# Kernel tuning notes

Hardware: AMD Instinct MI355X
Metric: run time of the kernel (lower is better)

## Reference

```python
import jax, jax.numpy as jnp
import numpy as np

IN_FEATURES = 256
OUT_FEATURES = 64
ALPHA = 0.2  # leaky relu slope


def _xavier_uniform(key, shape, gain=1.414):
    fan_in, fan_out = shape[0], shape[1]
    limit = gain * np.sqrt(6.0 / (fan_in + fan_out))
    return jax.random.uniform(key, shape, jnp.float32, -limit, limit)


def setup_inputs() -> dict:
    key = jax.random.key(0)
    k_h, k_W, k_a = jax.random.split(key, 3)
    h = jax.random.normal(k_h, (8, 2048, IN_FEATURES), dtype=jnp.float32)
    W = _xavier_uniform(k_W, (IN_FEATURES, OUT_FEATURES))
    a = _xavier_uniform(k_a, (2 * OUT_FEATURES, 1))
    return {"h": h, "W": W, "a": a}


def reference(h, W, a):
    # h: [B, N, F_in], W: [F_in, D], a: [2D, 1]
    Wh = h @ W  # [B, N, D]
    D = Wh.shape[-1]
    a1 = a[:D, 0]   # attends to source node i (repeat_interleave side)
    a2 = a[D:, 0]   # attends to target node j (repeat side)
    f1 = Wh @ a1    # [B, N]
    f2 = Wh @ a2    # [B, N]
    # e[b, i, j] = leakyrelu(a1.Wh[b,i] + a2.Wh[b,j])  -- identical math to
    # the original's O(N^2 * 2D) repeat/concat, without materializing it.
    e = jax.nn.leaky_relu(f1[:, :, None] + f2[:, None, :], negative_slope=ALPHA)  # [B, N, N]
    # NOTE: original applies softmax over dim=1 (over i, per column j).
    attention = jax.nn.softmax(e, axis=1)  # [B, N, N]
    # dropout is identity in eval mode
    h_prime = jnp.einsum('bij,bjd->bid', attention, Wh)  # [B, N, D]
    return jax.nn.elu(h_prime)  # concat=True path
```

## Files before the change

### kernel.cpp

```cpp
#include <hip/hip_runtime.h>

#define B 8
#define N 2048
#define KF 256
#define DF 64
#define LOG2E 1.44269504088896340736f
#define NR 2049

typedef __attribute__((ext_vector_type(8))) short short8;
typedef __attribute__((ext_vector_type(4))) float float4v;

__device__ __forceinline__ float fexp2(float x) {
#if __has_builtin(__builtin_amdgcn_exp2f)
    return __builtin_amdgcn_exp2f(x);
#else
    return exp2f(x);
#endif
}
__device__ __forceinline__ float eluf(float x) {
    return x > 0.f ? x : fexp2(x * LOG2E) - 1.0f;
}
__device__ __forceinline__ short bf16r(float x) {
    unsigned u = __float_as_uint(x);
    return (short)((u + 0x8000u) >> 16);
}
#define DOT4(c, u, p) \
    p = fmaf(c.x, u.x, fmaf(c.y, u.y, fmaf(c.z, u.z, fmaf(c.w, u.w, p))));

__global__ __launch_bounds__(256) void k_wh(const float* __restrict__ h,
                                            const float* __restrict__ W,
                                            const float* __restrict__ a,
                                            float* __restrict__ Wh,
                                            float* __restrict__ f1,
                                            float* __restrict__ f2) {
    __shared__ __align__(16) unsigned char smem[34816];
    short* lwt  = (short*)smem;
    float* lv   = (float*)(smem + 32768);
    float* lred = (float*)smem;
    float* lp   = (float*)(smem + 16896);

    int t = threadIdx.x;
    int wv = t >> 6, lane = t & 63;
    int n15 = lane & 15, q = lane >> 4;
    int bx = blockIdx.x;

    const float* hr = h + ((long)bx * 32 + n15) * KF + wv * 64 + q * 8;
    float4 c0 = *(const float4*)(hr);
    float4 c1 = *(const float4*)(hr + 4);
    float4 c2 = *(const float4*)(hr + 32);
    float4 c3 = *(const float4*)(hr + 36);

    {
        const float4* wr4 = (const float4*)(W + t * DF);
        float s1 = 0.f, s2 = 0.f;
        #pragma unroll
        for (int c = 0; c < 16; c++) {
            float4 w4 = wr4[c];
            float4 a1v = *(const float4*)(a + 4 * c);
            float4 a2v = *(const float4*)(a + DF + 4 * c);
            lwt[(4 * c + 0) * 256 + t] = bf16r(w4.x);
            lwt[(4 * c + 1) * 256 + t] = bf16r(w4.y);
            lwt[(4 * c + 2) * 256 + t] = bf16r(w4.z);
            lwt[(4 * c + 3) * 256 + t] = bf16r(w4.w);
            s1 = fmaf(w4.x, a1v.x, fmaf(w4.y, a1v.y, fmaf(w4.z, a1v.z, fmaf(w4.w, a1v.w, s1))));
            s2 = fmaf(w4.x, a2v.x, fmaf(w4.y, a2v.y, fmaf(w4.z, a2v.z, fmaf(w4.w, a2v.w, s2))));
        }
        lv[t] = s1;
        lv[256 + t] = s2;
    }
    __syncthreads();

    const short* bq = lwt + n15 * 256 + wv * 64 + q * 8;
    short8 s0b0 = *(const short8*)(bq);
    short8 s0b1 = *(const short8*)(bq + 16 * 256);
    short8 s0b2 = *(const short8*)(bq + 32 * 256);
    short8 s0b3 = *(const short8*)(bq + 48 * 256);
    short8 s1b0 = *(const short8*)(bq + 32);
    short8 s1b1 = *(const short8*)(bq + 16 * 256 + 32);
    short8 s1b2 = *(const short8*)(bq + 32 * 256 + 32);
    short8 s1b3 = *(const short8*)(bq + 48 * 256 + 32);
    const float* vv = lv + wv * 64 + q * 8;
    float4 u00 = *(const float4*)(vv);
    float4 u01 = *(const float4*)(vv + 4);
    float4 u10 = *(const float4*)(vv + 32);
    float4 u11 = *(const float4*)(vv + 36);
    float4 x00 = *(const float4*)(vv + 256);
    float4 x01 = *(const float4*)(vv + 256 + 4);
    float4 x10 = *(const float4*)(vv + 256 + 32);
    float4 x11 = *(const float4*)(vv + 256 + 36);
    __syncthreads();

    #pragma unroll
    for (int rt = 0; rt < 2; rt++) {
        float4 m0, m1, m2, m3;
        if (rt < 1) {
            const float* hn = hr + 16 * KF;
            m0 = *(const float4*)(hn);
            m1 = *(const float4*)(hn + 4);
            m2 = *(const float4*)(hn + 32);
            m3 = *(const float4*)(hn + 36);
        }
        float p1 = 0.f, p2 = 0.f;
        DOT4(c0, u00, p1) DOT4(c1, u01, p1) DOT4(c2, u10, p1) DOT4(c3, u11, p1)
        DOT4(c0, x00, p2) DOT4(c1, x01, p2) DOT4(c2, x10, p2) DOT4(c3, x11, p2)

        short8 af0 = { bf16r(c0.x), bf16r(c0.y), bf16r(c0.z), bf16r(c0.w),
                       bf16r(c1.x), bf16r(c1.y), bf16r(c1.z), bf16r(c1.w) };
        short8 af1 = { bf16r(c2.x), bf16r(c2.y), bf16r(c2.z), bf16r(c2.w),
                       bf16r(c3.x), bf16r(c3.y), bf16r(c3.z), bf16r(c3.w) };
        float4v acc0 = {0.f, 0.f, 0.f, 0.f}, acc1 = acc0, acc2 = acc0, acc3 = acc0;
        acc0 = __builtin_amdgcn_mfma_f32_16x16x32_bf16(af0, s0b0, acc0, 0, 0, 0);
        acc0 = __builtin_amdgcn_mfma_f32_16x16x32_bf16(af1, s1b0, acc0, 0, 0, 0);
        acc1 = __builtin_amdgcn_mfma_f32_16x16x32_bf16(af0, s0b1, acc1, 0, 0, 0);
        acc1 = __builtin_amdgcn_mfma_f32_16x16x32_bf16(af1, s1b1, acc1, 0, 0, 0);
        acc2 = __builtin_amdgcn_mfma_f32_16x16x32_bf16(af0, s0b2, acc2, 0, 0, 0);
        acc2 = __builtin_amdgcn_mfma_f32_16x16x32_bf16(af1, s1b2, acc2, 0, 0, 0);
        acc3 = __builtin_amdgcn_mfma_f32_16x16x32_bf16(af0, s0b3, acc3, 0, 0, 0);
        acc3 = __builtin_amdgcn_mfma_f32_16x16x32_bf16(af1, s1b3, acc3, 0, 0, 0);

        #define STASH(nb, A)                                                  \
            {                                                                 \
                _Pragma("unroll")                                             \
                for (int r = 0; r < 4; r++)                                   \
                    lred[wv * 1056 + (q * 4 + r) * 66 + nb * 16 + n15] = A[r]; \
            }
        STASH(0, acc0) STASH(1, acc1) STASH(2, acc2) STASH(3, acc3)
        #undef STASH
        p1 += __shfl_xor(p1, 16, 64); p1 += __shfl_xor(p1, 32, 64);
        p2 += __shfl_xor(p2, 16, 64); p2 += __shfl_xor(p2, 32, 64);
        if (q == 0) { lp[wv * 16 + n15] = p1; lp[64 + wv * 16 + n15] = p2; }
        __syncthreads();

        long i0 = (long)bx * 32 + rt * 16;
        int d = t & 63, ig = t >> 6;
        int bb = (int)(i0 >> 11);
        int il = (int)(i0 & (N - 1));
        float s0 = 0.f, s1 = 0.f, s2 = 0.f, s3 = 0.f;
        #pragma unroll
        for (int w = 0; w < 4; w++) {
            const float* lr = lred + w * 1056 + (ig * 4) * 66 + d;
            s0 += lr[0]; s1 += lr[66]; s2 += lr[132]; s3 += lr[198];
        }
        float* wp = Wh + ((long)bb * N + il + ig * 4) * DF + d;
        wp[0]      = s0;
        wp[DF]     = s1;
        wp[2 * DF] = s2;
        wp[3 * DF] = s3;

        if (t < 16) {
            f1[i0 + t] = lp[t] + lp[16 + t] + lp[32 + t] + lp[48 + t];
        } else if (t < 32) {
            int tt = t + 48;
            f2[i0 + t - 16] = lp[tt] + lp[16 + tt] + lp[32 + tt] + lp[48 + tt];
        }
        __syncthreads();
        c0 = m0; c1 = m1; c2 = m2; c3 = m3;
    }
}

__global__ __launch_bounds__(512) void k_rank(const float* __restrict__ f1,
                                              const float* __restrict__ f2,
                                              int* __restrict__ tIdx,
                                              int* __restrict__ si,
                                              float* __restrict__ gA,
                                              float* __restrict__ gsA) {
    __shared__ __align__(16) float4 qv[2048];
    __shared__ unsigned u2[2048];
    __shared__ float rS1[8][64], rS1s[8][64];
    __shared__ int   rC2[8][64], rC3[8][64];

    int t = threadIdx.x;
    int b = blockIdx.y;
    int base = blockIdx.x * 64;
    const float* f1g = f1 + b * N;
    const float* f2g = f2 + b * N;

    #pragma unroll
    for (int r = 0; r < 4; r++) {
        int idx = t + r * 512;
        float v1 = f1g[idx], v2 = f2g[idx];
        qv[idx] = make_float4(v1, fexp2(v1 * LOG2E), fexp2(v1 * 0.2f * LOG2E), v2);
        unsigned ub = __float_as_uint(v2);
        u2[idx] = ub ^ (((unsigned)((int)ub >> 31)) | 0x80000000u);
    }
    __syncthreads();

    int jl = t & 63, qt = t >> 6;
    int j = base + jl;
    float4 qj = qv[j];
    unsigned uj = u2[j];
    float negf2 = -qj.w, negf1 = -qj.x;
    int c2 = 0, c3 = 0;
    float S1 = 0.f, S1s = 0.f;
    int p0 = qt * 256;
    #pragma unroll 4
    for (int p = p0; p < p0 + 256; p++) {
        float4 qa = qv[p];
        unsigned up = u2[p];
        c2 += (up < uj || (up == uj && p < j)) ? 1 : 0;
        bool c = qa.x < negf2;
        S1  += c ? 0.f : qa.y;
        S1s += c ? qa.z : 0.f;
        c3 += (qa.w < negf1) ? 1 : 0;
    }
    rC2[qt][jl] = c2; rC3[qt][jl] = c3;
    rS1[qt][jl] = S1; rS1s[qt][jl] = S1s;
    __syncthreads();

    if (t < 64) {
        int j2 = base + t;
        float4 qj2 = qv[j2];
        int rank = 0, ti = 0;
        float s1 = 0.f, s1s = 0.f;
        #pragma unroll
        for (int k = 0; k < 8; k++) {
            rank += rC2[k][t]; ti += rC3[k][t];
            s1 += rS1[k][t];   s1s += rS1s[k][t];
        }
        float E2  = fexp2(qj2.w * LOG2E);
        float E2s = fexp2(qj2.w * 0.2f * LOG2E);
        float rr = 1.0f / (E2 * s1 + E2s * s1s);
        tIdx[b * N + j2] = ti;
        si [b * N + rank] = j2;
        gA [b * N + rank] = E2 * rr;
        gsA[b * N + rank] = E2s * rr;
    }
}

__global__ __launch_bounds__(256) void k_seg(const float* __restrict__ Wh,
                                             const int* __restrict__ si,
                                             const float* __restrict__ gA,
                                             const float* __restrict__ gsA,
                                             float* __restrict__ segG,
                                             float* __restrict__ segGs) {
    int t = threadIdx.x;
    int d = t & 63, sq = t >> 6;
    int seg = blockIdx.x * 4 + sq, b = blockIdx.y;
    const int*   sib = si  + b * N;
    const float* ga  = gA  + b * N;
    const float* gsa = gsA + b * N;
    const float* whb = Wh + (((long)b) << 11) * DF;
    float sg = 0.f, sgs = 0.f;
    #pragma unroll 8
    for (int x = 0; x < 32; x++) {
        int p = seg * 32 + x;
        int r = sib[p];
        float wv = whb[r * DF + d];
        sg  = fmaf(ga[p],  wv, sg);
        sgs = fmaf(gsa[p], wv, sgs);
    }
    segG [(b * 64 + seg) * DF + d] = sg;
    segGs[(b * 64 + seg) * DF + d] = sgs;
}

__global__ __launch_bounds__(256) void k_tab(const float* __restrict__ Wh,
                                             const int* __restrict__ si,
                                             const float* __restrict__ gA,
                                             const float* __restrict__ gsA,
                                             const float* __restrict__ segG,
                                             const float* __restrict__ segGs,
                                             float* __restrict__ SSg,
                                             float* __restrict__ PSgs) {
    __shared__ float lPG[4][64], lPGs[4][64];
    __shared__ float lTG[4][64], lTGs[4][64];
    __shared__ float wG[4][64],  wGs[4][64];
    int t = threadIdx.x;
    int d = t & 63, sub = t >> 6;
    int seg = blockIdx.x, b = blockIdx.y;

    const float* sgb  = segG  + (b * 64) * DF + d;
    const float* sgsb = segGs + (b * 64) * DF + d;
    float pg = 0.f, pgs = 0.f, tg = 0.f, tgs = 0.f;
    #pragma unroll
    for (int k = 0; k < 16; k++) {
        int s = sub * 16 + k;
        float vg = sgb[s * DF], vgs = sgsb[s * DF];
        tg += vg; tgs += vgs;
        if (s < seg) { pg += vg; pgs += vgs; }
    }
    lPG[sub][d] = pg; lPGs[sub][d] = pgs;
    lTG[sub][d] = tg; lTGs[sub][d] = tgs;

    int p0 = seg * 32 + sub * 8;
    const int*   sib = si  + b * N;
    const float* ga  = gA  + b * N;
    const float* gsa = gsA + b * N;
    const float* whb = Wh + (((long)b) << 11) * DF;
    float rows[8], gv[8], gsv[8];
    float sg = 0.f, sgs = 0.f;
    #pragma unroll
    for (int x = 0; x < 8; x++) {
        int p = p0 + x;
        int r = sib[p];
        float wv = whb[r * DF + d];
        rows[x] = wv; gv[x] = ga[p]; gsv[x] = gsa[p];
        sg  = fmaf(gv[x],  wv, sg);
        sgs = fmaf(gsv[x], wv, sgs);
    }
    wG[sub][d] = sg; wGs[sub][d] = sgs;
    __syncthreads();

    float totG  = lTG[0][d] + lTG[1][d] + lTG[2][d] + lTG[3][d];
    float totGs = lTGs[0][d] + lTGs[1][d] + lTGs[2][d] + lTGs[3][d];
    float baseG  = lPG[0][d] + lPG[1][d] + lPG[2][d] + lPG[3][d];
    float baseGs = lPGs[0][d] + lPGs[1][d] + lPGs[2][d] + lPGs[3][d];
    #pragma unroll
    for (int k = 0; k < 3; k++) {
        if (k < sub) { baseG += wG[k][d]; baseGs += wGs[k][d]; }
    }

    float* ssb = SSg  + ((long)b * NR) * DF + d;
    float* psb = PSgs + ((long)b * NR) * DF + d;
    float rg = baseG, rgs = baseGs;
    #pragma unroll
    for (int x = 0; x < 8; x++) {
        long p = p0 + x;
        ssb[p * DF] = totG - rg;
        psb[p * DF] = rgs;
        rg  = fmaf(gv[x],  rows[x], rg);
        rgs = fmaf(gsv[x], rows[x], rgs);
    }
    if (seg == 63 && sub == 3) {
        ssb[2048L * DF] = 0.f;
        psb[2048L * DF] = rgs;
    }
}

__global__ __launch_bounds__(256) void k_out(const float* __restrict__ f1,
                                             const int* __restrict__ tIdx,
                                             const float* __restrict__ SSg,
                                             const float* __restrict__ PSgs,
                                             float* __restrict__ out) {
    int t = threadIdx.x;
    int b = blockIdx.y;
    int i0 = blockIdx.x * 64;
    int rr = t >> 6, d = t & 63;
    const float* sgB = SSg  + ((long)b * NR) * DF + d;
    const float* pgB = PSgs + ((long)b * NR) * DF + d;
    float* ob = out + ((long)b * N + i0) * DF + d;
    #pragma unroll
    for (int kk = 0; kk < 16; kk++) {
        int r = rr + kk * 4;
        int ti = tIdx[b * N + i0 + r];
        float v = f1[b * N + i0 + r];
        float e1  = fexp2(v * LOG2E);
        float e1s = fexp2(v * 0.2f * LOG2E);
        float x = e1 * sgB[(long)ti * DF] + e1s * pgB[(long)ti * DF];
        ob[(long)r * DF] = eluf(x);
    }
}

extern "C" void kernel_launch(void* const* d_in, const int* in_sizes, int n_in,
                              void* d_out, int out_size, void* d_ws, size_t ws_size,
                              hipStream_t stream) {
    const float* h = (const float*)d_in[0];
    const float* W = (const float*)d_in[1];
    const float* a = (const float*)d_in[2];
    float* out = (float*)d_out;

    char* ws = (char*)d_ws;
    const size_t NB = (size_t)B * N;
    size_t off = 0;
    float* Wh    = (float*)(ws + off); off += NB * DF * sizeof(float);
    float* f1    = (float*)(ws + off); off += NB * sizeof(float);
    float* f2    = (float*)(ws + off); off += NB * sizeof(float);
    int*   tIdx  = (int*)  (ws + off); off += NB * sizeof(int);
    int*   si    = (int*)  (ws + off); off += NB * sizeof(int);
    float* gA    = (float*)(ws + off); off += NB * sizeof(float);
    float* gsA   = (float*)(ws + off); off += NB * sizeof(float);
    float* segG  = (float*)(ws + off); off += (size_t)B * 64 * DF * sizeof(float);
    float* segGs = (float*)(ws + off); off += (size_t)B * 64 * DF * sizeof(float);
    float* SSg   = (float*)(ws + off); off += (size_t)B * NR * DF * sizeof(float);
    float* PSgs  = (float*)(ws + off); off += (size_t)B * NR * DF * sizeof(float);
    (void)off; (void)ws_size;

    k_wh  <<<NB / 32, 256, 0, stream>>>(h, W, a, Wh, f1, f2);
    k_rank<<<dim3(N / 64, B), 512, 0, stream>>>(f1, f2, tIdx, si, gA, gsA);
    k_seg <<<dim3(16, B), 256, 0, stream>>>(Wh, si, gA, gsA, segG, segGs);
    k_tab <<<dim3(64, B), 256, 0, stream>>>(Wh, si, gA, gsA, segG, segGs, SSg, PSgs);
    k_out <<<dim3(N / 64, B), 256, 0, stream>>>(f1, tIdx, SSg, PSgs, out);
}
```

Before: 101.6 us.

## Fuse segment sums, prefix tables and output into one kernel

```diff
diff --git a/kernel.cpp b/kernel.cpp
--- a/kernel.cpp
+++ b/kernel.cpp
@@ -5,7 +5,6 @@
 #define KF 256
 #define DF 64
 #define LOG2E 1.44269504088896340736f
-#define NR 2049
 
 typedef __attribute__((ext_vector_type(8))) short short8;
 typedef __attribute__((ext_vector_type(4))) float float4v;
@@ -227,126 +226,80 @@
     }
 }
 
-__global__ __launch_bounds__(256) void k_seg(const float* __restrict__ Wh,
+__global__ __launch_bounds__(256) void k_fin(const float* __restrict__ Wh,
+                                             const float* __restrict__ f1,
+                                             const int* __restrict__ tIdx,
                                              const int* __restrict__ si,
                                              const float* __restrict__ gA,
                                              const float* __restrict__ gsA,
-                                             float* __restrict__ segG,
-                                             float* __restrict__ segGs) {
+                                             float* __restrict__ out) {
+    __shared__ int   lsi[2048];
+    __shared__ float lg[2048], lgs[2048];
+    __shared__ float pG[65][64], pGs[65][64];
+    __shared__ float e1v[64], e1sv[64];
+    __shared__ int   tv[64];
+
     int t = threadIdx.x;
-    int d = t & 63, sq = t >> 6;
-    int seg = blockIdx.x * 4 + sq, b = blockIdx.y;
-    const int*   sib = si  + b * N;
-    const float* ga  = gA  + b * N;
-    const float* gsa = gsA + b * N;
+    int d = t & 63, q = t >> 6;
+    int b = blockIdx.y, base = blockIdx.x * 64;
     const float* whb = Wh + (((long)b) << 11) * DF;
-    float sg = 0.f, sgs = 0.f;
-    #pragma unroll 8
-    for (int x = 0; x < 32; x++) {
-        int p = seg * 32 + x;
-        int r = sib[p];
-        float wv = whb[r * DF + d];
-        sg  = fmaf(ga[p],  wv, sg);
-        sgs = fmaf(gsa[p], wv, sgs);
-    }
-    segG [(b * 64 + seg) * DF + d] = sg;
-    segGs[(b * 64 + seg) * DF + d] = sgs;
-}
-
-__global__ __launch_bounds__(256) void k_tab(const float* __restrict__ Wh,
-                                             const int* __restrict__ si,
-                                             const float* __restrict__ gA,
-                                             const float* __restrict__ gsA,
-                                             const float* __restrict__ segG,
-                                             const float* __restrict__ segGs,
-                                             float* __restrict__ SSg,
-                                             float* __restrict__ PSgs) {
-    __shared__ float lPG[4][64], lPGs[4][64];
-    __shared__ float lTG[4][64], lTGs[4][64];
-    __shared__ float wG[4][64],  wGs[4][64];
-    int t = threadIdx.x;
-    int d = t & 63, sub = t >> 6;
-    int seg = blockIdx.x, b = blockIdx.y;
-
-    const float* sgb  = segG  + (b * 64) * DF + d;
-    const float* sgsb = segGs + (b * 64) * DF + d;
-    float pg = 0.f, pgs = 0.f, tg = 0.f, tgs = 0.f;
+
     #pragma unroll
-    for (int k = 0; k < 16; k++) {
-        int s = sub * 16 + k;
-        float vg = sgb[s * DF], vgs = sgsb[s * DF];
-        tg += vg; tgs += vgs;
-        if (s < seg) { pg += vg; pgs += vgs; }
-    }
-    lPG[sub][d] = pg; lPGs[sub][d] = pgs;
-    lTG[sub][d] = tg; lTGs[sub][d] = tgs;
-
-    int p0 = seg * 32 + sub * 8;
-    const int*   sib = si  + b * N;
-    const float* ga  = gA  + b * N;
-    const float* gsa = gsA + b * N;
-    const float* whb = Wh + (((long)b) << 11) * DF;
-    float rows[8], gv[8], gsv[8];
-    float sg = 0.f, sgs = 0.f;
-    #pragma unroll
-    for (int x = 0; x < 8; x++) {
-        int p = p0 + x;
-        int r = sib[p];
-        float wv = whb[r * DF + d];
-        rows[x] = wv; gv[x] = ga[p]; gsv[x] = gsa[p];
-        sg  = fmaf(gv[x],  wv, sg);
-        sgs = fmaf(gsv[x], wv, sgs);
-    }
-    wG[sub][d] = sg; wGs[sub][d] = sgs;
-    __syncthreads();
-
-    float totG  = lTG[0][d] + lTG[1][d] + lTG[2][d] + lTG[3][d];
-    float totGs = lTGs[0][d] + lTGs[1][d] + lTGs[2][d] + lTGs[3][d];
-    float baseG  = lPG[0][d] + lPG[1][d] + lPG[2][d] + lPG[3][d];
-    float baseGs = lPGs[0][d] + lPGs[1][d] + lPGs[2][d] + lPGs[3][d];
-    #pragma unroll
-    for (int k = 0; k < 3; k++) {
-        if (k < sub) { baseG += wG[k][d]; baseGs += wGs[k][d]; }
-    }
-
-    float* ssb = SSg  + ((long)b * NR) * DF + d;
-    float* psb = PSgs + ((long)b * NR) * DF + d;
-    float rg = baseG, rgs = baseGs;
-    #pragma unroll
-    for (int x = 0; x < 8; x++) {
-        long p = p0 + x;
-        ssb[p * DF] = totG - rg;
-        psb[p * DF] = rgs;
-        rg  = fmaf(gv[x],  rows[x], rg);
-        rgs = fmaf(gsv[x], rows[x], rgs);
-    }
-    if (seg == 63 && sub == 3) {
-        ssb[2048L * DF] = 0.f;
-        psb[2048L * DF] = rgs;
-    }
-}
-
-__global__ __launch_bounds__(256) void k_out(const float* __restrict__ f1,
-                                             const int* __restrict__ tIdx,
-                                             const float* __restrict__ SSg,
-                                             const float* __restrict__ PSgs,
-                                             float* __restrict__ out) {
-    int t = threadIdx.x;
-    int b = blockIdx.y;
-    int i0 = blockIdx.x * 64;
-    int rr = t >> 6, d = t & 63;
-    const float* sgB = SSg  + ((long)b * NR) * DF + d;
-    const float* pgB = PSgs + ((long)b * NR) * DF + d;
-    float* ob = out + ((long)b * N + i0) * DF + d;
-    #pragma unroll
-    for (int kk = 0; kk < 16; kk++) {
-        int r = rr + kk * 4;
-        int ti = tIdx[b * N + i0 + r];
-        float v = f1[b * N + i0 + r];
-        float e1  = fexp2(v * LOG2E);
-        float e1s = fexp2(v * 0.2f * LOG2E);
-        float x = e1 * sgB[(long)ti * DF] + e1s * pgB[(long)ti * DF];
-        ob[(long)r * DF] = eluf(x);
+    for (int r = 0; r < 8; r++) {
+        int p = t + r * 256;
+        lsi[p] = si[b * N + p];
+        lg[p]  = gA[b * N + p];
+        lgs[p] = gsA[b * N + p];
+    }
+    if (t < 64) {
+        int row = base + t;
+        float v = f1[b * N + row];
+        e1v[t]  = fexp2(v * LOG2E);
+        e1sv[t] = fexp2(v * 0.2f * LOG2E);
+        tv[t]   = tIdx[b * N + row];
+        pG[0][t] = 0.f; pGs[0][t] = 0.f;
+    }
+    __syncthreads();
+
+    #pragma unroll 1
+    for (int s = 0; s < 16; s++) {
+        int seg = q * 16 + s;
+        float sg = 0.f, sgs = 0.f;
+        #pragma unroll 8
+        for (int x = 0; x < 32; x++) {
+            int p = seg * 32 + x;
+            float w = whb[lsi[p] * DF + d];
+            sg  = fmaf(lg[p],  w, sg);
+            sgs = fmaf(lgs[p], w, sgs);
+        }
+        pG[seg + 1][d] = sg;
+        pGs[seg + 1][d] = sgs;
+    }
+    __syncthreads();
+    if (q == 0) {
+        float run = 0.f;
+        for (int s = 1; s <= 64; s++) { run += pG[s][d]; pG[s][d] = run; }
+    } else if (q == 1) {
+        float run = 0.f;
+        for (int s = 1; s <= 64; s++) { run += pGs[s][d]; pGs[s][d] = run; }
+    }
+    __syncthreads();
+
+    float TG = pG[64][d];
+    #pragma unroll 1
+    for (int rr = 0; rr < 16; rr++) {
+        int r = q * 16 + rr;
+        int ti = tv[r];
+        int s = ti >> 5, e = ti & 31, p0 = s * 32;
+        float pg = pG[s][d], pgs = pGs[s][d];
+        for (int x = 0; x < e; x++) {
+            int p = p0 + x;
+            float w = whb[lsi[p] * DF + d];
+            pg  = fmaf(lg[p],  w, pg);
+            pgs = fmaf(lgs[p], w, pgs);
+        }
+        float o = e1v[r] * (TG - pg) + e1sv[r] * pgs;
+        out[((long)b * N + base + r) * DF + d] = eluf(o);
     }
 }
 
@@ -361,22 +314,16 @@
     char* ws = (char*)d_ws;
     const size_t NB = (size_t)B * N;
     size_t off = 0;
-    float* Wh    = (float*)(ws + off); off += NB * DF * sizeof(float);
-    float* f1    = (float*)(ws + off); off += NB * sizeof(float);
-    float* f2    = (float*)(ws + off); off += NB * sizeof(float);
-    int*   tIdx  = (int*)  (ws + off); off += NB * sizeof(int);
-    int*   si    = (int*)  (ws + off); off += NB * sizeof(int);
-    float* gA    = (float*)(ws + off); off += NB * sizeof(float);
-    float* gsA   = (float*)(ws + off); off += NB * sizeof(float);
-    float* segG  = (float*)(ws + off); off += (size_t)B * 64 * DF * sizeof(float);
-    float* segGs = (float*)(ws + off); off += (size_t)B * 64 * DF * sizeof(float);
-    float* SSg   = (float*)(ws + off); off += (size_t)B * NR * DF * sizeof(float);
-    float* PSgs  = (float*)(ws + off); off += (size_t)B * NR * DF * sizeof(float);
+    float* Wh   = (float*)(ws + off); off += NB * DF * sizeof(float);
+    float* f1   = (float*)(ws + off); off += NB * sizeof(float);
+    float* f2   = (float*)(ws + off); off += NB * sizeof(float);
+    int*   tIdx = (int*)  (ws + off); off += NB * sizeof(int);
+    int*   si   = (int*)  (ws + off); off += NB * sizeof(int);
+    float* gA   = (float*)(ws + off); off += NB * sizeof(float);
+    float* gsA  = (float*)(ws + off); off += NB * sizeof(float);
     (void)off; (void)ws_size;
 
     k_wh  <<<NB / 32, 256, 0, stream>>>(h, W, a, Wh, f1, f2);
     k_rank<<<dim3(N / 64, B), 512, 0, stream>>>(f1, f2, tIdx, si, gA, gsA);
-    k_seg <<<dim3(16, B), 256, 0, stream>>>(Wh, si, gA, gsA, segG, segGs);
-    k_tab <<<dim3(64, B), 256, 0, stream>>>(Wh, si, gA, gsA, segG, segGs, SSg, PSgs);
-    k_out <<<dim3(N / 64, B), 256, 0, stream>>>(f1, tIdx, SSg, PSgs, out);
-}
+    k_fin <<<dim3(N / 64, B), 256, 0, stream>>>(Wh, f1, tIdx, si, gA, gsA, out);
+}
```

New measurement: 140.9 us. 1.39x slower.

## Fuse segment reduction into rank kernel via atomics and precompute packed sort keys

Applied to the files above, without the earlier changes.

```diff
diff --git a/kernel.cpp b/kernel.cpp
--- a/kernel.cpp
+++ b/kernel.cpp
@@ -24,6 +24,10 @@
     unsigned u = __float_as_uint(x);
     return (short)((u + 0x8000u) >> 16);
 }
+__device__ __forceinline__ unsigned sortkey(float x) {
+    unsigned u = __float_as_uint(x);
+    return u ^ (((unsigned)((int)u >> 31)) | 0x80000000u);
+}
 #define DOT4(c, u, p) \
     p = fmaf(c.x, u.x, fmaf(c.y, u.y, fmaf(c.z, u.z, fmaf(c.w, u.w, p))));
 
@@ -32,7 +36,9 @@
                                             const float* __restrict__ a,
                                             float* __restrict__ Wh,
                                             float* __restrict__ f1,
-                                            float* __restrict__ f2) {
+                                            float* __restrict__ f2,
+                                            float4* __restrict__ qpack,
+                                            float* __restrict__ segzero) {
     __shared__ __align__(16) unsigned char smem[34816];
     short* lwt  = (short*)smem;
     float* lv   = (float*)(smem + 32768);
@@ -43,6 +49,8 @@
     int wv = t >> 6, lane = t & 63;
     int n15 = lane & 15, q = lane >> 4;
     int bx = blockIdx.x;
+
+    if (t < 128) segzero[bx * 128 + t] = 0.f;
 
     const float* hr = h + ((long)bx * 32 + n15) * KF + wv * 64 + q * 8;
     float4 c0 = *(const float4*)(hr);
@@ -148,7 +156,15 @@
         wp[3 * DF] = s3;
 
         if (t < 16) {
-            f1[i0 + t] = lp[t] + lp[16 + t] + lp[32 + t] + lp[48 + t];
+            float v1 = lp[t] + lp[16 + t] + lp[32 + t] + lp[48 + t];
+            f1[i0 + t] = v1;
+            float v2 = lp[64 + t] + lp[80 + t] + lp[96 + t] + lp[112 + t];
+            float4 qe;
+            qe.x = __uint_as_float(sortkey(v1));
+            qe.y = __uint_as_float(sortkey(v2));
+            qe.z = fexp2(v1 * LOG2E);
+            qe.w = fexp2(v1 * 0.2f * LOG2E);
+            qpack[i0 + t] = qe;
         } else if (t < 32) {
             int tt = t + 48;
             f2[i0 + t - 16] = lp[tt] + lp[16 + tt] + lp[32 + tt] + lp[48 + tt];
@@ -158,58 +174,54 @@
     }
 }
 
-__global__ __launch_bounds__(512) void k_rank(const float* __restrict__ f1,
+__global__ __launch_bounds__(512) void k_rank(const float4* __restrict__ qpack,
+                                              const float* __restrict__ f1,
                                               const float* __restrict__ f2,
+                                              const float* __restrict__ Wh,
                                               int* __restrict__ tIdx,
                                               int* __restrict__ si,
                                               float* __restrict__ gA,
-                                              float* __restrict__ gsA) {
-    __shared__ __align__(16) float4 qv[2048];
-    __shared__ unsigned u2[2048];
+                                              float* __restrict__ gsA,
+                                              float* __restrict__ segG,
+                                              float* __restrict__ segGs) {
     __shared__ float rS1[8][64], rS1s[8][64];
     __shared__ int   rC2[8][64], rC3[8][64];
+    __shared__ float gL[64], gsL[64];
+    __shared__ int   rkL[64];
 
     int t = threadIdx.x;
-    int b = blockIdx.y;
-    int base = blockIdx.x * 64;
-    const float* f1g = f1 + b * N;
-    const float* f2g = f2 + b * N;
-
-    #pragma unroll
-    for (int r = 0; r < 4; r++) {
-        int idx = t + r * 512;
-        float v1 = f1g[idx], v2 = f2g[idx];
-        qv[idx] = make_float4(v1, fexp2(v1 * LOG2E), fexp2(v1 * 0.2f * LOG2E), v2);
-        unsigned ub = __float_as_uint(v2);
-        u2[idx] = ub ^ (((unsigned)((int)ub >> 31)) | 0x80000000u);
-    }
-    __syncthreads();
-
-    int jl = t & 63, qt = t >> 6;
+    int b = blockIdx.y, base = blockIdx.x * 64;
+    int jl = t & 63;
     int j = base + jl;
-    float4 qj = qv[j];
-    unsigned uj = u2[j];
-    float negf2 = -qj.w, negf1 = -qj.x;
+    float f1j = f1[(long)b * N + j];
+    float f2j = f2[(long)b * N + j];
+    unsigned u2j = sortkey(f2j);
+    unsigned long long Kj = (((unsigned long long)u2j) << 32) | (unsigned)j;
+    unsigned vkNf2 = sortkey(-f2j);
+    unsigned vkNf1 = sortkey(-f1j);
+
+    int qt = __builtin_amdgcn_readfirstlane(t >> 6);
+    const float4* qp = qpack + (long)b * N + qt * 256;
     int c2 = 0, c3 = 0;
     float S1 = 0.f, S1s = 0.f;
-    int p0 = qt * 256;
-    #pragma unroll 4
-    for (int p = p0; p < p0 + 256; p++) {
-        float4 qa = qv[p];
-        unsigned up = u2[p];
-        c2 += (up < uj || (up == uj && p < j)) ? 1 : 0;
-        bool c = qa.x < negf2;
-        S1  += c ? 0.f : qa.y;
-        S1s += c ? qa.z : 0.f;
-        c3 += (qa.w < negf1) ? 1 : 0;
+    #pragma unroll 8
+    for (int x = 0; x < 256; x++) {
+        float4 e = qp[x];
+        unsigned u1p = __float_as_uint(e.x);
+        unsigned u2p = __float_as_uint(e.y);
+        unsigned long long Kp = (((unsigned long long)u2p) << 32)
+                              | (unsigned)(qt * 256 + x);
+        c2 += (Kp < Kj) ? 1 : 0;
+        c3 += (u2p < vkNf1) ? 1 : 0;
+        bool cc = u1p < vkNf2;
+        S1  += cc ? 0.f : e.z;
+        S1s += cc ? e.w : 0.f;
     }
     rC2[qt][jl] = c2; rC3[qt][jl] = c3;
     rS1[qt][jl] = S1; rS1s[qt][jl] = S1s;
     __syncthreads();
 
     if (t < 64) {
-        int j2 = base + t;
-        float4 qj2 = qv[j2];
         int rank = 0, ti = 0;
         float s1 = 0.f, s1s = 0.f;
         #pragma unroll
@@ -217,40 +229,29 @@
             rank += rC2[k][t]; ti += rC3[k][t];
             s1 += rS1[k][t];   s1s += rS1s[k][t];
         }
-        float E2  = fexp2(qj2.w * LOG2E);
-        float E2s = fexp2(qj2.w * 0.2f * LOG2E);
+        float E2  = fexp2(f2j * LOG2E);
+        float E2s = fexp2(f2j * 0.2f * LOG2E);
         float rr = 1.0f / (E2 * s1 + E2s * s1s);
-        tIdx[b * N + j2] = ti;
-        si [b * N + rank] = j2;
-        gA [b * N + rank] = E2 * rr;
-        gsA[b * N + rank] = E2s * rr;
-    }
-}
-
-__global__ __launch_bounds__(256) void k_seg(const float* __restrict__ Wh,
-                                             const int* __restrict__ si,
-                                             const float* __restrict__ gA,
-                                             const float* __restrict__ gsA,
-                                             float* __restrict__ segG,
-                                             float* __restrict__ segGs) {
-    int t = threadIdx.x;
-    int d = t & 63, sq = t >> 6;
-    int seg = blockIdx.x * 4 + sq, b = blockIdx.y;
-    const int*   sib = si  + b * N;
-    const float* ga  = gA  + b * N;
-    const float* gsa = gsA + b * N;
+        float g = E2 * rr, gs = E2s * rr;
+        tIdx[(long)b * N + j] = ti;
+        si [(long)b * N + rank] = j;
+        gA [(long)b * N + rank] = g;
+        gsA[(long)b * N + rank] = gs;
+        rkL[t] = rank; gL[t] = g; gsL[t] = gs;
+    }
+    __syncthreads();
+
+    int d = t & 63, rg = t >> 6;
     const float* whb = Wh + (((long)b) << 11) * DF;
-    float sg = 0.f, sgs = 0.f;
-    #pragma unroll 8
-    for (int x = 0; x < 32; x++) {
-        int p = seg * 32 + x;
-        int r = sib[p];
-        float wv = whb[r * DF + d];
-        sg  = fmaf(ga[p],  wv, sg);
-        sgs = fmaf(gsa[p], wv, sgs);
-    }
-    segG [(b * 64 + seg) * DF + d] = sg;
-    segGs[(b * 64 + seg) * DF + d] = sgs;
+    #pragma unroll
+    for (int r = 0; r < 8; r++) {
+        int lr = rg * 8 + r;
+        int row = base + lr;
+        float w = whb[row * DF + d];
+        int seg = rkL[lr] >> 5;
+        atomicAdd(&segG [(b * 64 + seg) * DF + d], gL[lr] * w);
+        atomicAdd(&segGs[(b * 64 + seg) * DF + d], gsL[lr] * w);
+    }
 }
 
 __global__ __launch_bounds__(256) void k_tab(const float* __restrict__ Wh,
@@ -301,7 +302,6 @@
     __syncthreads();
 
     float totG  = lTG[0][d] + lTG[1][d] + lTG[2][d] + lTG[3][d];
-    float totGs = lTGs[0][d] + lTGs[1][d] + lTGs[2][d] + lTGs[3][d];
     float baseG  = lPG[0][d] + lPG[1][d] + lPG[2][d] + lPG[3][d];
     float baseGs = lPGs[0][d] + lPGs[1][d] + lPGs[2][d] + lPGs[3][d];
     #pragma unroll
@@ -361,22 +361,22 @@
     char* ws = (char*)d_ws;
     const size_t NB = (size_t)B * N;
     size_t off = 0;
-    float* Wh    = (float*)(ws + off); off += NB * DF * sizeof(float);
-    float* f1    = (float*)(ws + off); off += NB * sizeof(float);
-    float* f2    = (float*)(ws + off); off += NB * sizeof(float);
-    int*   tIdx  = (int*)  (ws + off); off += NB * sizeof(int);
-    int*   si    = (int*)  (ws + off); off += NB * sizeof(int);
-    float* gA    = (float*)(ws + off); off += NB * sizeof(float);
-    float* gsA   = (float*)(ws + off); off += NB * sizeof(float);
-    float* segG  = (float*)(ws + off); off += (size_t)B * 64 * DF * sizeof(float);
-    float* segGs = (float*)(ws + off); off += (size_t)B * 64 * DF * sizeof(float);
-    float* SSg   = (float*)(ws + off); off += (size_t)B * NR * DF * sizeof(float);
-    float* PSgs  = (float*)(ws + off); off += (size_t)B * NR * DF * sizeof(float);
+    float*  Wh    = (float*) (ws + off); off += NB * DF * sizeof(float);
+    float*  f1    = (float*) (ws + off); off += NB * sizeof(float);
+    float*  f2    = (float*) (ws + off); off += NB * sizeof(float);
+    int*    tIdx  = (int*)   (ws + off); off += NB * sizeof(int);
+    int*    si    = (int*)   (ws + off); off += NB * sizeof(int);
+    float*  gA    = (float*) (ws + off); off += NB * sizeof(float);
+    float*  gsA   = (float*) (ws + off); off += NB * sizeof(float);
+    float4* qpack = (float4*)(ws + off); off += NB * sizeof(float4);
+    float*  segG  = (float*) (ws + off); off += (size_t)B * 64 * DF * sizeof(float);
+    float*  segGs = (float*) (ws + off); off += (size_t)B * 64 * DF * sizeof(float);
+    float*  SSg   = (float*) (ws + off); off += (size_t)B * NR * DF * sizeof(float);
+    float*  PSgs  = (float*) (ws + off); off += (size_t)B * NR * DF * sizeof(float);
     (void)off; (void)ws_size;
 
-    k_wh  <<<NB / 32, 256, 0, stream>>>(h, W, a, Wh, f1, f2);
-    k_rank<<<dim3(N / 64, B), 512, 0, stream>>>(f1, f2, tIdx, si, gA, gsA);
-    k_seg <<<dim3(16, B), 256, 0, stream>>>(Wh, si, gA, gsA, segG, segGs);
+    k_wh  <<<NB / 32, 256, 0, stream>>>(h, W, a, Wh, f1, f2, qpack, segG);
+    k_rank<<<dim3(N / 64, B), 512, 0, stream>>>(qpack, f1, f2, Wh, tIdx, si, gA, gsA, segG, segGs);
     k_tab <<<dim3(64, B), 256, 0, stream>>>(Wh, si, gA, gsA, segG, segGs, SSg, PSgs);
     k_out <<<dim3(N / 64, B), 256, 0, stream>>>(f1, tIdx, SSg, PSgs, out);
 }
```

Measured after the change: 114.9 us. 13.2% more time.

## Fuse output pass into prefix table kernel by bucketing rows by threshold

Applied to the files above, without the earlier changes.

```diff
diff --git a/kernel.cpp b/kernel.cpp
--- a/kernel.cpp
+++ b/kernel.cpp
@@ -23,6 +23,10 @@
 __device__ __forceinline__ short bf16r(float x) {
     unsigned u = __float_as_uint(x);
     return (short)((u + 0x8000u) >> 16);
+}
+__device__ __forceinline__ unsigned sortkey(float x) {
+    unsigned u = __float_as_uint(x);
+    return u ^ (((unsigned)((int)u >> 31)) | 0x80000000u);
 }
 #define DOT4(c, u, p) \
     p = fmaf(c.x, u.x, fmaf(c.y, u.y, fmaf(c.z, u.z, fmaf(c.w, u.w, p))));
@@ -160,28 +164,29 @@
 
 __global__ __launch_bounds__(512) void k_rank(const float* __restrict__ f1,
                                               const float* __restrict__ f2,
-                                              int* __restrict__ tIdx,
                                               int* __restrict__ si,
                                               float* __restrict__ gA,
-                                              float* __restrict__ gsA) {
+                                              float* __restrict__ gsA,
+                                              int* __restrict__ s1i,
+                                              float2* __restrict__ e1pk,
+                                              int* __restrict__ Rarr) {
     __shared__ __align__(16) float4 qv[2048];
     __shared__ unsigned u2[2048];
     __shared__ float rS1[8][64], rS1s[8][64];
-    __shared__ int   rC2[8][64], rC3[8][64];
+    __shared__ int   rC1[8][64], rC2[8][64], rC4[8][64];
 
     int t = threadIdx.x;
     int b = blockIdx.y;
     int base = blockIdx.x * 64;
-    const float* f1g = f1 + b * N;
-    const float* f2g = f2 + b * N;
+    const float* f1g = f1 + (long)b * N;
+    const float* f2g = f2 + (long)b * N;
 
     #pragma unroll
     for (int r = 0; r < 4; r++) {
         int idx = t + r * 512;
         float v1 = f1g[idx], v2 = f2g[idx];
         qv[idx] = make_float4(v1, fexp2(v1 * LOG2E), fexp2(v1 * 0.2f * LOG2E), v2);
-        unsigned ub = __float_as_uint(v2);
-        u2[idx] = ub ^ (((unsigned)((int)ub >> 31)) | 0x80000000u);
+        u2[idx] = sortkey(v2);
     }
     __syncthreads();
 
@@ -189,41 +194,47 @@
     int j = base + jl;
     float4 qj = qv[j];
     unsigned uj = u2[j];
-    float negf2 = -qj.w, negf1 = -qj.x;
-    int c2 = 0, c3 = 0;
+    unsigned u1j = sortkey(qj.x);
+    float negf2 = -qj.w;
+    int c1 = 0, c2 = 0, c4 = 0;
     float S1 = 0.f, S1s = 0.f;
     int p0 = qt * 256;
     #pragma unroll 4
     for (int p = p0; p < p0 + 256; p++) {
         float4 qa = qv[p];
         unsigned up = u2[p];
+        unsigned u1p = sortkey(qa.x);
         c2 += (up < uj || (up == uj && p < j)) ? 1 : 0;
-        bool c = qa.x < negf2;
-        S1  += c ? 0.f : qa.y;
-        S1s += c ? qa.z : 0.f;
-        c3 += (qa.w < negf1) ? 1 : 0;
-    }
-    rC2[qt][jl] = c2; rC3[qt][jl] = c3;
+        c1 += (u1p > u1j || (u1p == u1j && p < j)) ? 1 : 0;
+        bool cc = qa.x < negf2;
+        c4 += cc ? 1 : 0;
+        S1  += cc ? 0.f : qa.y;
+        S1s += cc ? qa.z : 0.f;
+    }
+    rC1[qt][jl] = c1; rC2[qt][jl] = c2; rC4[qt][jl] = c4;
     rS1[qt][jl] = S1; rS1s[qt][jl] = S1s;
     __syncthreads();
 
     if (t < 64) {
         int j2 = base + t;
         float4 qj2 = qv[j2];
-        int rank = 0, ti = 0;
+        int rank1 = 0, rank2 = 0, cnt4 = 0;
         float s1 = 0.f, s1s = 0.f;
         #pragma unroll
         for (int k = 0; k < 8; k++) {
-            rank += rC2[k][t]; ti += rC3[k][t];
-            s1 += rS1[k][t];   s1s += rS1s[k][t];
+            rank1 += rC1[k][t]; rank2 += rC2[k][t]; cnt4 += rC4[k][t];
+            s1 += rS1[k][t];    s1s += rS1s[k][t];
         }
         float E2  = fexp2(qj2.w * LOG2E);
         float E2s = fexp2(qj2.w * 0.2f * LOG2E);
         float rr = 1.0f / (E2 * s1 + E2s * s1s);
-        tIdx[b * N + j2] = ti;
-        si [b * N + rank] = j2;
-        gA [b * N + rank] = E2 * rr;
-        gsA[b * N + rank] = E2s * rr;
+        si [(long)b * N + rank2] = j2;
+        gA [(long)b * N + rank2] = E2 * rr;
+        gsA[(long)b * N + rank2] = E2s * rr;
+        Rarr[(long)b * NR + rank2 + 1] = N - cnt4;
+        s1i [(long)b * N + rank1] = j2;
+        e1pk[(long)b * N + rank1] = make_float2(qj2.y, qj2.z);
+        if (blockIdx.x == 0 && t == 0) Rarr[(long)b * NR] = 0;
     }
 }
 
@@ -236,9 +247,9 @@
     int t = threadIdx.x;
     int d = t & 63, sq = t >> 6;
     int seg = blockIdx.x * 4 + sq, b = blockIdx.y;
-    const int*   sib = si  + b * N;
-    const float* ga  = gA  + b * N;
-    const float* gsa = gsA + b * N;
+    const int*   sib = si  + (long)b * N;
+    const float* ga  = gA  + (long)b * N;
+    const float* gsa = gsA + (long)b * N;
     const float* whb = Wh + (((long)b) << 11) * DF;
     float sg = 0.f, sgs = 0.f;
     #pragma unroll 8
@@ -253,16 +264,18 @@
     segGs[(b * 64 + seg) * DF + d] = sgs;
 }
 
-__global__ __launch_bounds__(256) void k_tab(const float* __restrict__ Wh,
-                                             const int* __restrict__ si,
-                                             const float* __restrict__ gA,
-                                             const float* __restrict__ gsA,
-                                             const float* __restrict__ segG,
-                                             const float* __restrict__ segGs,
-                                             float* __restrict__ SSg,
-                                             float* __restrict__ PSgs) {
+__global__ __launch_bounds__(256) void k_tabout(const float* __restrict__ Wh,
+                                                const int* __restrict__ si,
+                                                const float* __restrict__ gA,
+                                                const float* __restrict__ gsA,
+                                                const float* __restrict__ segG,
+                                                const float* __restrict__ segGs,
+                                                const int* __restrict__ s1i,
+                                                const float2* __restrict__ e1pk,
+                                                const int* __restrict__ Rarr,
+                                                float* __restrict__ out) {
     __shared__ float lPG[4][64], lPGs[4][64];
-    __shared__ float lTG[4][64], lTGs[4][64];
+    __shared__ float lTG[4][64];
     __shared__ float wG[4][64],  wGs[4][64];
     int t = threadIdx.x;
     int d = t & 63, sub = t >> 6;
@@ -270,21 +283,21 @@
 
     const float* sgb  = segG  + (b * 64) * DF + d;
     const float* sgsb = segGs + (b * 64) * DF + d;
-    float pg = 0.f, pgs = 0.f, tg = 0.f, tgs = 0.f;
+    float pg = 0.f, pgs = 0.f, tg = 0.f;
     #pragma unroll
     for (int k = 0; k < 16; k++) {
         int s = sub * 16 + k;
         float vg = sgb[s * DF], vgs = sgsb[s * DF];
-        tg += vg; tgs += vgs;
+        tg += vg;
         if (s < seg) { pg += vg; pgs += vgs; }
     }
     lPG[sub][d] = pg; lPGs[sub][d] = pgs;
-    lTG[sub][d] = tg; lTGs[sub][d] = tgs;
+    lTG[sub][d] = tg;
 
     int p0 = seg * 32 + sub * 8;
-    const int*   sib = si  + b * N;
-    const float* ga  = gA  + b * N;
-    const float* gsa = gsA + b * N;
+    const int*   sib = si  + (long)b * N;
+    const float* ga  = gA  + (long)b * N;
+    const float* gsa = gsA + (long)b * N;
     const float* whb = Wh + (((long)b) << 11) * DF;
     float rows[8], gv[8], gsv[8];
     float sg = 0.f, sgs = 0.f;
@@ -300,8 +313,7 @@
     wG[sub][d] = sg; wGs[sub][d] = sgs;
     __syncthreads();
 
-    float totG  = lTG[0][d] + lTG[1][d] + lTG[2][d] + lTG[3][d];
-    float totGs = lTGs[0][d] + lTGs[1][d] + lTGs[2][d] + lTGs[3][d];
+    float totG   = lTG[0][d] + lTG[1][d] + lTG[2][d] + lTG[3][d];
     float baseG  = lPG[0][d] + lPG[1][d] + lPG[2][d] + lPG[3][d];
     float baseGs = lPGs[0][d] + lPGs[1][d] + lPGs[2][d] + lPGs[3][d];
     #pragma unroll
@@ -309,44 +321,35 @@
         if (k < sub) { baseG += wG[k][d]; baseGs += wGs[k][d]; }
     }
 
-    float* ssb = SSg  + ((long)b * NR) * DF + d;
-    float* psb = PSgs + ((long)b * NR) * DF + d;
+    const int*    Ra = Rarr + (long)b * NR;
+    const int*    s1b = s1i + (long)b * N;
+    const float2* e1b = e1pk + (long)b * N;
+    float* ob = out + ((long)b * N) * DF + d;
+
     float rg = baseG, rgs = baseGs;
     #pragma unroll
     for (int x = 0; x < 8; x++) {
-        long p = p0 + x;
-        ssb[p * DF] = totG - rg;
-        psb[p * DF] = rgs;
+        int p = p0 + x;
+        float ss = totG - rg;
+        float ps = rgs;
+        int r0 = __builtin_amdgcn_readfirstlane(Ra[p]);
+        int r1 = __builtin_amdgcn_readfirstlane(Ra[p + 1]);
+        for (int rr = r0; rr < r1; rr++) {
+            int row = s1b[rr];
+            float2 ee = e1b[rr];
+            ob[(long)row * DF] = eluf(ee.x * ss + ee.y * ps);
+        }
         rg  = fmaf(gv[x],  rows[x], rg);
         rgs = fmaf(gsv[x], rows[x], rgs);
     }
     if (seg == 63 && sub == 3) {
-        ssb[2048L * DF] = 0.f;
-        psb[2048L * DF] = rgs;
-    }
-}
-
-__global__ __launch_bounds__(256) void k_out(const float* __restrict__ f1,
-                                             const int* __restrict__ tIdx,
-                                             const float* __restrict__ SSg,
-                                             const float* __restrict__ PSgs,
-                                             float* __restrict__ out) {
-    int t = threadIdx.x;
-    int b = blockIdx.y;
-    int i0 = blockIdx.x * 64;
-    int rr = t >> 6, d = t & 63;
-    const float* sgB = SSg  + ((long)b * NR) * DF + d;
-    const float* pgB = PSgs + ((long)b * NR) * DF + d;
-    float* ob = out + ((long)b * N + i0) * DF + d;
-    #pragma unroll
-    for (int kk = 0; kk < 16; kk++) {
-        int r = rr + kk * 4;
-        int ti = tIdx[b * N + i0 + r];
-        float v = f1[b * N + i0 + r];
-        float e1  = fexp2(v * LOG2E);
-        float e1s = fexp2(v * 0.2f * LOG2E);
-        float x = e1 * sgB[(long)ti * DF] + e1s * pgB[(long)ti * DF];
-        ob[(long)r * DF] = eluf(x);
+        float ps = rgs;
+        int r0 = __builtin_amdgcn_readfirstlane(Ra[2048]);
+        for (int rr = r0; rr < N; rr++) {
+            int row = s1b[rr];
+            float2 ee = e1b[rr];
+            ob[(long)row * DF] = eluf(ee.y * ps);
+        }
     }
 }
 
@@ -361,22 +364,22 @@
     char* ws = (char*)d_ws;
     const size_t NB = (size_t)B * N;
     size_t off = 0;
-    float* Wh    = (float*)(ws + off); off += NB * DF * sizeof(float);
-    float* f1    = (float*)(ws + off); off += NB * sizeof(float);
-    float* f2    = (float*)(ws + off); off += NB * sizeof(float);
-    int*   tIdx  = (int*)  (ws + off); off += NB * sizeof(int);
-    int*   si    = (int*)  (ws + off); off += NB * sizeof(int);
-    float* gA    = (float*)(ws + off); off += NB * sizeof(float);
-    float* gsA   = (float*)(ws + off); off += NB * sizeof(float);
-    float* segG  = (float*)(ws + off); off += (size_t)B * 64 * DF * sizeof(float);
-    float* segGs = (float*)(ws + off); off += (size_t)B * 64 * DF * sizeof(float);
-    float* SSg   = (float*)(ws + off); off += (size_t)B * NR * DF * sizeof(float);
-    float* PSgs  = (float*)(ws + off); off += (size_t)B * NR * DF * sizeof(float);
+    float*  Wh    = (float*) (ws + off); off += NB * DF * sizeof(float);
+    float*  f1    = (float*) (ws + off); off += NB * sizeof(float);
+    float*  f2    = (float*) (ws + off); off += NB * sizeof(float);
+    float*  gA    = (float*) (ws + off); off += NB * sizeof(float);
+    float*  gsA   = (float*) (ws + off); off += NB * sizeof(float);
+    float2* e1pk  = (float2*)(ws + off); off += NB * sizeof(float2);
+    int*    si    = (int*)   (ws + off); off += NB * sizeof(int);
+    int*    s1i   = (int*)   (ws + off); off += NB * sizeof(int);
+    int*    Rarr  = (int*)   (ws + off); off += (size_t)B * NR * sizeof(int);
+    float*  segG  = (float*) (ws + off); off += (size_t)B * 64 * DF * sizeof(float);
+    float*  segGs = (float*) (ws + off); off += (size_t)B * 64 * DF * sizeof(float);
     (void)off; (void)ws_size;
 
-    k_wh  <<<NB / 32, 256, 0, stream>>>(h, W, a, Wh, f1, f2);
-    k_rank<<<dim3(N / 64, B), 512, 0, stream>>>(f1, f2, tIdx, si, gA, gsA);
-    k_seg <<<dim3(16, B), 256, 0, stream>>>(Wh, si, gA, gsA, segG, segGs);
-    k_tab <<<dim3(64, B), 256, 0, stream>>>(Wh, si, gA, gsA, segG, segGs, SSg, PSgs);
-    k_out <<<dim3(N / 64, B), 256, 0, stream>>>(f1, tIdx, SSg, PSgs, out);
-}
+    k_wh    <<<NB / 32, 256, 0, stream>>>(h, W, a, Wh, f1, f2);
+    k_rank  <<<dim3(N / 64, B), 512, 0, stream>>>(f1, f2, si, gA, gsA, s1i, e1pk, Rarr);
+    k_seg   <<<dim3(16, B), 256, 0, stream>>>(Wh, si, gA, gsA, segG, segGs);
+    k_tabout<<<dim3(64, B), 256, 0, stream>>>(Wh, si, gA, gsA, segG, segGs,
+                                              s1i, e1pk, Rarr, out);
+}
```

Result: slower. 112.2 us (+10.5%).
